# Optimization experiments

Hardware: AMD Instinct MI355X
Metric: run time of the kernel (lower is better)

Reference implementation:

```python
import jax, jax.numpy as jnp
import numpy as np

N_NODES = 49
FEAT_DIM = 1280            # efficientnet_v2_s feature dim
NODE_DIM = FEAT_DIM // N_NODES  # 26
GAT_HID = 256
HEADS = 4
NUM_CLASSES = 5
BATCH = 8192


def _grid_edges():
    # 7x7 grid, 8-neighborhood, as in _create_grid_edges, plus PyG default self loops
    edges = []
    for i in range(7):
        for j in range(7):
            node = i * 7 + j
            for di in (-1, 0, 1):
                for dj in (-1, 0, 1):
                    if di == 0 and dj == 0:
                        continue
                    ni, nj = i + di, j + dj
                    if 0 <= ni < 7 and 0 <= nj < 7:
                        edges.append((node, ni * 7 + nj))
    edges += [(n, n) for n in range(N_NODES)]  # add_self_loops=True (PyG default)
    return np.asarray(edges, dtype=np.int64).T  # [2, 361]


def setup_inputs() -> dict:
    key = jax.random.key(0)
    ks = jax.random.split(key, 16)
    s = 0.05
    inp = {
        "x": jax.random.normal(ks[0], (BATCH, FEAT_DIM), jnp.float32),
        "transform_w": jax.random.normal(ks[1], (FEAT_DIM, N_NODES * NODE_DIM), jnp.float32) * s,
        "transform_b": jnp.zeros((N_NODES * NODE_DIM,), jnp.float32),
        # GATv2 layer 1: 26 -> 64 per head, 4 heads, concat -> 256
        "g1_wl": jax.random.normal(ks[2], (NODE_DIM, GAT_HID), jnp.float32) * s,
        "g1_wr": jax.random.normal(ks[3], (NODE_DIM, GAT_HID), jnp.float32) * s,
        "g1_att": jax.random.normal(ks[4], (HEADS, GAT_HID // HEADS), jnp.float32) * s,
        "g1_b": jnp.zeros((GAT_HID,), jnp.float32),
        # GATv2 layer 2: 256 -> 256, 1 head, mean
        "g2_wl": jax.random.normal(ks[5], (GAT_HID, GAT_HID), jnp.float32) * s,
        "g2_wr": jax.random.normal(ks[6], (GAT_HID, GAT_HID), jnp.float32) * s,
        "g2_att": jax.random.normal(ks[7], (1, GAT_HID), jnp.float32) * s,
        "g2_b": jnp.zeros((GAT_HID,), jnp.float32),
        "fc_w": jax.random.normal(ks[8], (NODE_DIM + GAT_HID, NUM_CLASSES), jnp.float32) * s,
        "fc_b": jnp.zeros((NUM_CLASSES,), jnp.float32),
        "edge_index": jnp.asarray(_grid_edges()),
    }
    return inp


def _gatv2(x, src, dst, wl, wr, att, b, heads, out_ch, concat):
    # PyG GATv2Conv (share_weights=False, negative_slope=0.2, eval mode)
    n = x.shape[0]
    xl = (x @ wl).reshape(n, heads, out_ch)  # source messages
    xr = (x @ wr).reshape(n, heads, out_ch)  # target side of attention
    e = jax.nn.leaky_relu(xl[src] + xr[dst], 0.2)        # [E, H, C]
    score = jnp.einsum('ehc,hc->eh', e, att)             # [E, H]
    smax = jax.ops.segment_max(score, dst, num_segments=n)
    ex = jnp.exp(score - smax[dst])
    den = jax.ops.segment_sum(ex, dst, num_segments=n)
    alpha = ex / den[dst]                                # softmax over in-edges per node
    out = jax.ops.segment_sum(xl[src] * alpha[..., None], dst, num_segments=n)  # [N,H,C]
    out = out.reshape(n, heads * out_ch) if concat else out.mean(axis=1)
    return out + b


def reference(x, transform_w, transform_b, g1_wl, g1_wr, g1_att, g1_b,
              g2_wl, g2_wr, g2_att, g2_b, fc_w, fc_b, edge_index):
    src, dst = edge_index[0], edge_index[1]
    node = (x @ transform_w + transform_b).reshape(-1, N_NODES, NODE_DIM)  # [B,49,26]

    def graph(nf):
        h = _gatv2(nf, src, dst, g1_wl, g1_wr, g1_att, g1_b, HEADS, GAT_HID // HEADS, True)
        h = jax.nn.elu(h)  # dropout inactive in eval
        h = _gatv2(h, src, dst, g2_wl, g2_wr, g2_att, g2_b, 1, GAT_HID, False)
        return h  # [49, 256]

    g = jax.vmap(graph)(node)                              # [B,49,256]
    pooled = jnp.concatenate([node, g], axis=-1).mean(axis=1)  # [B, 282]
    return pooled @ fc_w + fc_b
```

## Files before the change

### kernel.cpp

```cpp
#include <hip/hip_runtime.h>
#include <hip/hip_bf16.h>

typedef __bf16 bf16;
typedef __attribute__((ext_vector_type(8))) __bf16 bf16x8;
typedef __attribute__((ext_vector_type(4))) __bf16 bf16x4;
typedef __attribute__((ext_vector_type(4))) float f32x4;

constexpr int BATCH = 8192, NN = 49, ND = 26, NOUT = 1274, FD = 1280;
constexpr int HID = 256, NE = 361, HEADS = 4;
constexpr int KT_X = 40;
constexpr int MT_X = 512;
constexpr int NB_W = 10;
constexpr int NTB  = 9;

constexpr size_t OFF_XPACK = 0;
constexpr size_t SZ_XPACK  = (size_t)MT_X * KT_X * 512 * 2;
constexpr size_t OFF_WPACK = OFF_XPACK + SZ_XPACK;
constexpr size_t SZ_WPACK  = (size_t)NB_W * NTB * KT_X * 512 * 2;
constexpr size_t OFF_B1    = OFF_WPACK + SZ_WPACK;
constexpr size_t SZ_B1     = (size_t)32 * 512 * 2;
constexpr size_t OFF_B2    = OFF_B1 + SZ_B1;
constexpr size_t SZ_B2     = (size_t)32 * 8 * 512 * 2;
constexpr size_t OFF_N32   = OFF_B2 + SZ_B2;
constexpr size_t SZ_N32    = (size_t)BATCH * NN * 32 * 2;
constexpr size_t OFF_PN    = OFF_N32 + SZ_N32;
constexpr size_t SZ_PN     = (size_t)BATCH * ND * 4;
constexpr size_t OFF_CSR   = OFF_PN + SZ_PN;
constexpr size_t SZ_CSR    = 8192;
constexpr size_t OFF_CHUNK = OFF_CSR + SZ_CSR;


__global__ __launch_bounds__(256) void k_pack_x(const float* __restrict__ x,
                                                bf16* __restrict__ xp) {
    int g = blockIdx.x * 256 + threadIdx.x;
    int lane = g & 63, frag = g >> 6;
    int mt = frag / KT_X, kt = frag - mt * KT_X;
    int row = mt * 16 + (lane & 15);
    int k0  = kt * 32 + (lane >> 4) * 8;
    const float* src = x + (size_t)row * FD + k0;
    bf16x8 v;
#pragma unroll
    for (int j = 0; j < 8; ++j) v[j] = (bf16)src[j];
    *(bf16x8*)(xp + ((size_t)frag * 64 + lane) * 8) = v;
}

__global__ __launch_bounds__(256) void k_pack_w(const float* __restrict__ w,
                                                bf16* __restrict__ wp) {
    int g = blockIdx.x * 256 + threadIdx.x;
    int lane = g & 63, frag = g >> 6;
    int kt = frag % KT_X, t2 = frag / KT_X;
    int nt = t2 % NTB, nb = t2 / NTB;
    int col = nb * 130 + nt * 16 + (lane & 15);
    int k0  = kt * 32 + (lane >> 4) * 8;
    bool ok = (col < NOUT) && (col < nb * 130 + 130);
    bf16x8 v;
#pragma unroll
    for (int j = 0; j < 8; ++j)
        v[j] = ok ? (bf16)w[(size_t)(k0 + j) * NOUT + col] : (bf16)0.f;
    *(bf16x8*)(wp + ((size_t)frag * 64 + lane) * 8) = v;
}

__global__ __launch_bounds__(256) void k_pack_g1(const float* __restrict__ wl,
                                                 const float* __restrict__ wr,
                                                 bf16* __restrict__ bp) {
    int g = blockIdx.x * 256 + threadIdx.x;
    int lane = g & 63, nt = g >> 6;
    int n  = nt * 16 + (lane & 15);
    int k0 = (lane >> 4) * 8;
    bf16x8 v;
#pragma unroll
    for (int j = 0; j < 8; ++j) {
        int k = k0 + j;
        float f = 0.f;
        if (k < ND) f = (n < HID) ? wl[k * HID + n] : wr[k * HID + (n - HID)];
        v[j] = (bf16)f;
    }
    *(bf16x8*)(bp + ((size_t)nt * 64 + lane) * 8) = v;
}

__global__ __launch_bounds__(256) void k_pack_g2(const float* __restrict__ wl,
                                                 const float* __restrict__ wr,
                                                 bf16* __restrict__ bp) {
    int g = blockIdx.x * 256 + threadIdx.x;
    int lane = g & 63, frag = g >> 6;
    int nt = frag >> 3, kt = frag & 7;
    int n  = nt * 16 + (lane & 15);
    int k0 = kt * 32 + (lane >> 4) * 8;
    bf16x8 v;
#pragma unroll
    for (int j = 0; j < 8; ++j) {
        int k = k0 + j;
        float f = (n < HID) ? wl[k * HID + n] : wr[k * HID + (n - HID)];
        v[j] = (bf16)f;
    }
    *(bf16x8*)(bp + ((size_t)frag * 64 + lane) * 8) = v;
}

__global__ __launch_bounds__(128) void k_csr_par(const int* __restrict__ ei,
                                                 int* __restrict__ csr) {
    __shared__ int es[NE], ed[NE], cnt[NN], ocnt[NN], off[NN + 1], ooff[NN + 1];
    int tid = threadIdx.x;
    if (tid < NN) { cnt[tid] = 0; ocnt[tid] = 0; }
    for (int e = tid; e < NE; e += 128) { es[e] = ei[e]; ed[e] = ei[NE + e]; }
    __syncthreads();
    for (int e = tid; e < NE; e += 128) {
        atomicAdd(&cnt[ed[e]], 1);
        atomicAdd(&ocnt[es[e]], 1);
    }
    __syncthreads();
    if (tid == 0) {
        off[0] = 0; ooff[0] = 0;
        for (int n = 0; n < NN; ++n) {
            off[n + 1] = off[n] + cnt[n];
            ooff[n + 1] = ooff[n] + ocnt[n];
        }
    }
    __syncthreads();
    if (tid < NN) {
        int p = off[tid];
        for (int e = 0; e < NE; ++e)
            if (ed[e] == tid) { csr[50 + p] = e; csr[411 + p] = es[e]; ++p; }
    } else if (tid >= 64 && tid < 64 + NN) {
        int n = tid - 64;
        int p = ooff[n];
        for (int e = 0; e < NE; ++e)
            if (es[e] == n) { csr[822 + p] = e; ++p; }
    }
    if (tid < 50) { csr[tid] = off[tid]; csr[772 + tid] = ooff[tid]; }
}

__global__ __launch_bounds__(256, 2) void k_gemm_node(const bf16* __restrict__ xp,
                                                      const bf16* __restrict__ wp,
                                                      const float* __restrict__ tb,
                                                      bf16* __restrict__ node32) {
    __shared__ bf16 L[128][148];
    __shared__ float tbS[144];
    int tid = threadIdx.x, lane = tid & 63, w = tid >> 6;
    int nb = blockIdx.y, C0 = nb * 130;
    int mt0 = blockIdx.x * 16 + w * 4;
    if (tid < 144) { int col = C0 + tid; tbS[tid] = (col < NOUT) ? tb[col] : 0.f; }
    f32x4 acc[4][9] = {};
    const bf16* wpB = wp + (size_t)(nb * NTB) * KT_X * 512;
    for (int kt = 0; kt < KT_X; ++kt) {
        bf16x8 a[4];
#pragma unroll
        for (int i = 0; i < 4; ++i)
            a[i] = *(const bf16x8*)(xp + (((size_t)(mt0 + i) * KT_X + kt) * 64 + lane) * 8);
#pragma unroll
        for (int j = 0; j < NTB; ++j) {
            bf16x8 b = *(const bf16x8*)(wpB + ((size_t)(j * KT_X + kt) * 64 + lane) * 8);
#pragma unroll
            for (int i = 0; i < 4; ++i)
                acc[i][j] = __builtin_amdgcn_mfma_f32_16x16x32_bf16(a[i], b, acc[i][j], 0, 0, 0);
        }
    }
    int c0 = lane & 15, r0 = (lane >> 4) * 4;
    int nodes = (nb == 9) ? 4 : 5;
    int total = 128 * nodes * 4;
    for (int half = 0; half < 2; ++half) {
        __syncthreads();
        if ((w >> 1) == half) {
            int lrbase = (w & 1) * 64;
#pragma unroll
            for (int i = 0; i < 4; ++i) {
#pragma unroll
                for (int j = 0; j < NTB; ++j) {
                    int col = j * 16 + c0;
                    float bias = tbS[col];
#pragma unroll
                    for (int r = 0; r < 4; ++r)
                        L[lrbase + i * 16 + r0 + r][col] = (bf16)(acc[i][j][r] + bias);
                }
            }
        }
        __syncthreads();
        int B0 = blockIdx.x * 256 + half * 128;
        for (int t = tid; t < total; t += 256) {
            int q = t & 3, t2 = t >> 2;
            int n_l = t2 % nodes, brow = t2 / nodes;
            bf16x8 o;
#pragma unroll
            for (int jj = 0; jj < 8; ++jj) {
                int d = q * 8 + jj;
                o[jj] = (d < ND) ? L[brow][n_l * 26 + d] : (bf16)0.f;
            }
            *(bf16x8*)(node32 + (((size_t)(B0 + brow) * NN + nb * 5 + n_l) * 32 + q * 8)) = o;
        }
    }
}

__global__ __launch_bounds__(256) void k_pool(const bf16* __restrict__ node32,
                                              float* __restrict__ pN) {
    int b = blockIdx.x * 8 + (threadIdx.x >> 5);
    int d = threadIdx.x & 31;
    if (d >= ND) return;
    const bf16* base = node32 + (size_t)b * NN * 32 + d;
    float s = 0.f;
    for (int n = 0; n < NN; ++n) s += (float)base[n * 32];
    pN[b * ND + d] = s;
}

__global__ __launch_bounds__(512, 2) void k_fuse1(const bf16* __restrict__ n32,
                                                  const bf16* __restrict__ B1p,
                                                  bf16* __restrict__ h1f,
                                                  const float* __restrict__ att1,
                                                  const float* __restrict__ g1b,
                                                  const int* __restrict__ ei,
                                                  const int* __restrict__ csr) {
    __shared__ __align__(16) char X[NN * 1024];
    __shared__ __align__(16) float attS[256];
    __shared__ float sc[NE * 4], srden[NN * 4], bS[256];
    __shared__ int ieOff[50], ieId[NE], ieSrc[NE], srcS[NE], dstS[NE];

    int tid = threadIdx.x, lane = tid & 63, w = tid >> 6, g = blockIdx.x;

    for (int i = tid; i < 256; i += 512) { attS[i] = att1[i]; bS[i] = g1b[i]; }
    for (int i = tid; i < NE; i += 512) {
        srcS[i] = ei[i]; dstS[i] = ei[NE + i];
        ieId[i] = csr[50 + i]; ieSrc[i] = csr[411 + i];
    }
    if (tid < 50) ieOff[tid] = csr[tid];

    {
        int mt = w & 3, ng = w >> 2;
        int m = mt * 16 + (lane & 15);
        bf16x8 bfrag = {};
        if (m < NN)
            bfrag = *(const bf16x8*)(n32 + ((size_t)(g * NN + m) * 32 + (lane >> 4) * 8));
        int chq = (lane >> 4) * 4;
        int sw = (m & 7) << 4;
        char* rowp = X + m * 1024;
#pragma unroll
        for (int j = 0; j < 16; ++j) {
            f32x4 z = {0.f, 0.f, 0.f, 0.f};
            bf16x8 afrag = *(const bf16x8*)(B1p + ((size_t)(ng * 16 + j) * 64 + lane) * 8);
            f32x4 acc = __builtin_amdgcn_mfma_f32_16x16x32_bf16(afrag, bfrag, z, 0, 0, 0);
            if (m < NN) {
                int ch = (ng * 16 + j) * 16 + chq;
                bf16x4 o4;
#pragma unroll
                for (int r = 0; r < 4; ++r) o4[r] = (bf16)acc[r];
                *(bf16x4*)(rowp + ((ch * 2) ^ sw)) = o4;
            }
        }
    }
    __syncthreads();

    int rot = tid & 7;
    for (int task = tid; task < NE * 4; task += 512) {
        int h = task / NE, e = task - h * NE;
        int s = srcS[e], d = dstS[e];
        int sws = (s & 7) << 4, swd = (d & 7) << 4;
        const char* ps = X + s * 1024;
        const char* pd = X + d * 1024;
        float pa[4] = {0.f, 0.f, 0.f, 0.f};
#pragma unroll
        for (int i = 0; i < 8; ++i) {
            int cc = ((i + rot) & 7) * 8;
            bf16x8 xl = *(const bf16x8*)(ps + (((h * 64 + cc) * 2) ^ sws));
            bf16x8 xr = *(const bf16x8*)(pd + (((256 + h * 64 + cc) * 2) ^ swd));
            float4 a0 = *(const float4*)(attS + h * 64 + cc);
            float4 a1 = *(const float4*)(attS + h * 64 + cc + 4);
            const float aa[8] = {a0.x, a0.y, a0.z, a0.w, a1.x, a1.y, a1.z, a1.w};
#pragma unroll
            for (int q = 0; q < 8; ++q) {
                float v = (float)xl[q] + (float)xr[q];
                v = v > 0.f ? v : 0.2f * v;
                pa[q & 3] = fmaf(aa[q], v, pa[q & 3]);
            }
        }
        sc[e * 4 + h] = (pa[0] + pa[1]) + (pa[2] + pa[3]);
    }
    __syncthreads();
    for (int t = tid; t < NN * 4; t += 512) {
        int n = t >> 2, h = t & 3;
        float m = -1e30f;
        for (int j = ieOff[n]; j < ieOff[n + 1]; ++j) m = fmaxf(m, sc[ieId[j] * 4 + h]);
        float den = 0.f;
        for (int j = ieOff[n]; j < ieOff[n + 1]; ++j) {
            int idx = ieId[j] * 4 + h;
            float ex = __expf(sc[idx] - m);
            sc[idx] = ex; den += ex;
        }
        srden[t] = 1.f / den;
    }
    __syncthreads();
    for (int task = tid; task < NN * 32; task += 512) {
        int n = task >> 5, cb = task & 31;
        int ch0 = cb * 8, hh = cb >> 3;
        float a8[8] = {};
        int j0 = ieOff[n], j1 = ieOff[n + 1];
        for (int j = j0; j < j1; ++j) {
            float al = sc[ieId[j] * 4 + hh];
            int s = ieSrc[j];
            bf16x8 xv = *(const bf16x8*)(X + s * 1024 + ((ch0 * 2) ^ ((s & 7) << 4)));
#pragma unroll
            for (int q = 0; q < 8; ++q) a8[q] = fmaf(al, (float)xv[q], a8[q]);
        }
        float rs = srden[n * 4 + hh];
        bf16x8 o;
#pragma unroll
        for (int q = 0; q < 8; ++q) {
            float v = fmaf(a8[q], rs, bS[ch0 + q]);
            v = v > 0.f ? v : (__expf(v) - 1.f);
            o[q] = (bf16)v;
        }
        int Rl = g * NN + n;
        int kt = ch0 >> 5, kg = (ch0 >> 3) & 3;
        size_t addr = (((size_t)(Rl >> 4) * 8 + kt) * 64 + (Rl & 15) + 16 * kg) * 8;
        *(bf16x8*)(h1f + addr) = o;
    }
}

__global__ __launch_bounds__(256) void k_gemm_l2(const bf16* __restrict__ Af,
                                                 const bf16* __restrict__ Bf,
                                                 bf16* __restrict__ xlr) {
    __shared__ bf16 LT[128][136];
    int tid = threadIdx.x, lane = tid & 63, w = tid >> 6;
    int mtb = blockIdx.x * 8 + (w >> 1) * 4;
    int ntb = blockIdx.y * 8 + (w & 1) * 4;
    f32x4 acc[4][4] = {};
    for (int kt = 0; kt < 8; ++kt) {
        bf16x8 a[4], b[4];
#pragma unroll
        for (int i = 0; i < 4; ++i)
            a[i] = *(const bf16x8*)(Af + (((size_t)(mtb + i) * 8 + kt) * 64 + lane) * 8);
#pragma unroll
        for (int j = 0; j < 4; ++j)
            b[j] = *(const bf16x8*)(Bf + (((size_t)(ntb + j) * 8 + kt) * 64 + lane) * 8);
#pragma unroll
        for (int i = 0; i < 4; ++i)
#pragma unroll
            for (int j = 0; j < 4; ++j)
                acc[i][j] = __builtin_amdgcn_mfma_f32_16x16x32_bf16(a[i], b[j], acc[i][j], 0, 0, 0);
    }
    int c0 = lane & 15, r0 = (lane >> 4) * 4;
    int lr0 = (w >> 1) * 64, lc0 = (w & 1) * 64;
#pragma unroll
    for (int i = 0; i < 4; ++i)
#pragma unroll
        for (int j = 0; j < 4; ++j)
#pragma unroll
            for (int r = 0; r < 4; ++r)
                LT[lr0 + i * 16 + r0 + r][lc0 + j * 16 + c0] = (bf16)acc[i][j][r];
    __syncthreads();
    size_t R0 = (size_t)blockIdx.x * 128, C0 = (size_t)blockIdx.y * 128;
#pragma unroll
    for (int it = 0; it < 8; ++it) {
        int idx = (it * 256 + tid) * 8;
        int r = idx >> 7, c = idx & 127;
        bf16x8 v = *(const bf16x8*)&LT[r][c];
        *(bf16x8*)(xlr + (R0 + r) * 512 + C0 + c) = v;
    }
}

__global__ __launch_bounds__(384) void k_score2(const bf16* __restrict__ xlr,
                                                const float* __restrict__ att2,
                                                const int* __restrict__ ei,
                                                float* __restrict__ scE) {
    __shared__ __align__(16) char X[NN * 1024];
    __shared__ float attS[256];
    int tid = threadIdx.x, g = blockIdx.x;
    const char* srcp = (const char*)(xlr + (size_t)g * NN * 512);
    for (int off = tid * 16; off < NN * 1024; off += 384 * 16) {
        int row = off >> 10;
        *(uint4*)(X + (off ^ ((row & 7) << 4))) = *(const uint4*)(srcp + off);
    }
    if (tid < 256) attS[tid] = att2[tid];
    __syncthreads();
    if (tid >= NE) return;
    int s = ei[tid], d = ei[NE + tid];
    int sws = (s & 7) << 4, swd = (d & 7) << 4;
    const char* ps = X + s * 1024;
    const char* pd = X + d * 1024;
    int rot = tid & 7;
    float pa[4] = {0.f, 0.f, 0.f, 0.f};
#pragma unroll 8
    for (int i = 0; i < 32; ++i) {
        int cc = ((i + rot) & 31) * 8;
        bf16x8 xl = *(const bf16x8*)(ps + ((cc * 2) ^ sws));
        bf16x8 xr = *(const bf16x8*)(pd + (((256 + cc) * 2) ^ swd));
        float4 a0 = *(const float4*)(attS + cc);
        float4 a1 = *(const float4*)(attS + cc + 4);
        const float aa[8] = {a0.x, a0.y, a0.z, a0.w, a1.x, a1.y, a1.z, a1.w};
#pragma unroll
        for (int q = 0; q < 8; ++q) {
            float v = (float)xl[q] + (float)xr[q];
            v = v > 0.f ? v : 0.2f * v;
            pa[q & 3] = fmaf(aa[q], v, pa[q & 3]);
        }
    }
    scE[(size_t)g * NE + tid] = (pa[0] + pa[1]) + (pa[2] + pa[3]);
}

__global__ __launch_bounds__(64) void k_softwn(const float* __restrict__ scE,
                                               const int* __restrict__ csr,
                                               const int* __restrict__ ei,
                                               float* __restrict__ wN) {
    __shared__ float sm[NN], sr[NN];
    int g = blockIdx.x, tid = threadIdx.x;
    const float* sg = scE + (size_t)g * NE;
    if (tid < NN) {
        int j0 = csr[tid], j1 = csr[tid + 1];
        float m = -1e30f;
        for (int j = j0; j < j1; ++j) m = fmaxf(m, sg[csr[50 + j]]);
        float den = 0.f;
        for (int j = j0; j < j1; ++j) den += __expf(sg[csr[50 + j]] - m);
        sm[tid] = m; sr[tid] = 1.f / den;
    }
    __syncthreads();
    if (tid < NN) {
        float wa = 0.f;
        int j0 = csr[772 + tid], j1 = csr[772 + tid + 1];
        for (int j = j0; j < j1; ++j) {
            int e = csr[822 + j];
            int d = ei[NE + e];
            wa += __expf(sg[e] - sm[d]) * sr[d];
        }
        wN[(size_t)g * NN + tid] = wa;
    }
}

static __device__ __forceinline__ float waveReduceSum(float v) {
#pragma unroll
    for (int m = 32; m > 0; m >>= 1) v += __shfl_xor(v, m, 64);
    return v;
}

__global__ __launch_bounds__(256) void k_poolfc(const bf16* __restrict__ xlr,
                                                const float* __restrict__ wN,
                                                const float* __restrict__ pN,
                                                const float* __restrict__ g2b,
                                                const float* __restrict__ fcw,
                                                const float* __restrict__ fcb,
                                                int graph_base,
                                                float* __restrict__ out) {
    __shared__ float wSs[NN];
    __shared__ float poolS[288];
    int tid = threadIdx.x, g = blockIdx.x;
    if (tid < NN) wSs[tid] = wN[(size_t)g * NN + tid];
    if (tid >= 64 && tid < 64 + ND)
        poolS[tid - 64] = pN[(size_t)(graph_base + g) * ND + (tid - 64)] * (1.f / NN);
    __syncthreads();
    {
        const bf16* base = xlr + (size_t)g * NN * 512 + tid;
        float acc = 0.f;
        for (int n = 0; n < NN; ++n) acc = fmaf(wSs[n], (float)base[n * 512], acc);
        poolS[ND + tid] = acc * (1.f / NN) + g2b[tid];
    }
    __syncthreads();
    int w5 = tid >> 6, lane = tid & 63;
    for (int o = w5; o < 5; o += 4) {
        float a = 0.f;
        for (int d = lane; d < ND + HID; d += 64) a = fmaf(poolS[d], fcw[d * 5 + o], a);
        a = waveReduceSum(a);
        if (lane == 0) out[(size_t)(graph_base + g) * 5 + o] = a + fcb[o];
    }
}

extern "C" void kernel_launch(void* const* d_in, const int* in_sizes, int n_in,
                              void* d_out, int out_size, void* d_ws, size_t ws_size,
                              hipStream_t stream) {
    const float* x   = (const float*)d_in[0];
    const float* tw  = (const float*)d_in[1];
    const float* tb  = (const float*)d_in[2];
    const float* wl1 = (const float*)d_in[3];
    const float* wr1 = (const float*)d_in[4];
    const float* at1 = (const float*)d_in[5];
    const float* b1  = (const float*)d_in[6];
    const float* wl2 = (const float*)d_in[7];
    const float* wr2 = (const float*)d_in[8];
    const float* at2 = (const float*)d_in[9];
    const float* b2  = (const float*)d_in[10];
    const float* fcw = (const float*)d_in[11];
    const float* fcb = (const float*)d_in[12];
    const int*   ei  = (const int*)d_in[13];
    float* out = (float*)d_out;

    char* ws = (char*)d_ws;
    bf16*  xp   = (bf16*)(ws + OFF_XPACK);
    bf16*  wp   = (bf16*)(ws + OFF_WPACK);
    bf16*  b1p  = (bf16*)(ws + OFF_B1);
    bf16*  b2p  = (bf16*)(ws + OFF_B2);
    bf16*  n32  = (bf16*)(ws + OFF_N32);
    float* pN   = (float*)(ws + OFF_PN);
    int*   csr  = (int*)(ws + OFF_CSR);

    const size_t perC = 50176 + 12544 + 1444 + 196;
    int C = 512;
    for (int cand : {2048, 1024, 512}) {
        if (OFF_CHUNK + (size_t)cand * perC <= ws_size) { C = cand; break; }
    }
    bf16*  xlr = (bf16*)(ws + OFF_CHUNK);
    bf16*  h1f = (bf16*)(ws + OFF_CHUNK + (size_t)C * 50176);
    float* scE = (float*)(ws + OFF_CHUNK + (size_t)C * (50176 + 12544));
    float* wNB = scE + (size_t)C * NE;
    int nchunks = BATCH / C;
    int MtC = C * NN / 16;

    k_pack_x<<<dim3(MT_X * KT_X * 64 / 256), dim3(256), 0, stream>>>(x, xp);
    k_pack_w<<<dim3(NB_W * NTB * KT_X * 64 / 256), dim3(256), 0, stream>>>(tw, wp);
    k_pack_g1<<<dim3(8), dim3(256), 0, stream>>>(wl1, wr1, b1p);
    k_pack_g2<<<dim3(64), dim3(256), 0, stream>>>(wl2, wr2, b2p);
    k_csr_par<<<dim3(1), dim3(128), 0, stream>>>(ei, csr);
    k_gemm_node<<<dim3(32, NB_W), dim3(256), 0, stream>>>(xp, wp, tb, n32);
    k_pool<<<dim3(BATCH / 8), dim3(256), 0, stream>>>(n32, pN);

    for (int c = 0; c < nchunks; ++c) {
        const bf16* n32c = n32 + (size_t)c * C * NN * 32;
        k_fuse1<<<dim3(C), dim3(512), 0, stream>>>(n32c, b1p, h1f, at1, b1, ei, csr);
        k_gemm_l2<<<dim3(MtC / 8, 4), dim3(256), 0, stream>>>(h1f, b2p, xlr);
        k_score2<<<dim3(C), dim3(384), 0, stream>>>(xlr, at2, ei, scE);
        k_softwn<<<dim3(C), dim3(64), 0, stream>>>(scE, csr, ei, wNB);
        k_poolfc<<<dim3(C), dim3(256), 0, stream>>>(xlr, wNB, pN, b2, fcw, fcb,
                                                    c * C, out);
    }
}
```

Baseline: 944.0 us.

## Aggregate layer-1 attention via dense MFMA matrix and fuse softmax into score2

```diff
diff --git a/kernel.cpp b/kernel.cpp
--- a/kernel.cpp
+++ b/kernel.cpp
@@ -119,7 +119,7 @@
     if (tid < NN) {
         int p = off[tid];
         for (int e = 0; e < NE; ++e)
-            if (ed[e] == tid) { csr[50 + p] = e; csr[411 + p] = es[e]; ++p; }
+            if (ed[e] == tid) { csr[50 + p] = e; csr[411 + p] = es[e]; csr[1200 + p] = tid; ++p; }
     } else if (tid >= 64 && tid < 64 + NN) {
         int n = tid - 64;
         int p = ooff[n];
@@ -205,19 +205,18 @@
                                                   bf16* __restrict__ h1f,
                                                   const float* __restrict__ att1,
                                                   const float* __restrict__ g1b,
-                                                  const int* __restrict__ ei,
                                                   const int* __restrict__ csr) {
     __shared__ __align__(16) char X[NN * 1024];
+    __shared__ __align__(16) bf16 P2[2][64][72];
     __shared__ __align__(16) float attS[256];
-    __shared__ float sc[NE * 4], srden[NN * 4], bS[256];
-    __shared__ int ieOff[50], ieId[NE], ieSrc[NE], srcS[NE], dstS[NE];
+    __shared__ float sc2[NE * 2], bS[256];
+    __shared__ int ieOff[50], ieDst[NE], ieSrc[NE];
 
     int tid = threadIdx.x, lane = tid & 63, w = tid >> 6, g = blockIdx.x;
 
     for (int i = tid; i < 256; i += 512) { attS[i] = att1[i]; bS[i] = g1b[i]; }
     for (int i = tid; i < NE; i += 512) {
-        srcS[i] = ei[i]; dstS[i] = ei[NE + i];
-        ieId[i] = csr[50 + i]; ieSrc[i] = csr[411 + i];
+        ieDst[i] = csr[1200 + i]; ieSrc[i] = csr[411 + i];
     }
     if (tid < 50) ieOff[tid] = csr[tid];
 
@@ -246,62 +245,97 @@
     }
     __syncthreads();
 
-    int rot = tid & 7;
-    for (int task = tid; task < NE * 4; task += 512) {
-        int h = task / NE, e = task - h * NE;
-        int s = srcS[e], d = dstS[e];
-        int sws = (s & 7) << 4, swd = (d & 7) << 4;
-        const char* ps = X + s * 1024;
-        const char* pd = X + d * 1024;
-        float pa[4] = {0.f, 0.f, 0.f, 0.f};
-#pragma unroll
-        for (int i = 0; i < 8; ++i) {
-            int cc = ((i + rot) & 7) * 8;
-            bf16x8 xl = *(const bf16x8*)(ps + (((h * 64 + cc) * 2) ^ sws));
-            bf16x8 xr = *(const bf16x8*)(pd + (((256 + h * 64 + cc) * 2) ^ swd));
-            float4 a0 = *(const float4*)(attS + h * 64 + cc);
-            float4 a1 = *(const float4*)(attS + h * 64 + cc + 4);
-            const float aa[8] = {a0.x, a0.y, a0.z, a0.w, a1.x, a1.y, a1.z, a1.w};
-#pragma unroll
-            for (int q = 0; q < 8; ++q) {
-                float v = (float)xl[q] + (float)xr[q];
-                v = v > 0.f ? v : 0.2f * v;
-                pa[q & 3] = fmaf(aa[q], v, pa[q & 3]);
-            }
-        }
-        sc[e * 4 + h] = (pa[0] + pa[1]) + (pa[2] + pa[3]);
-    }
-    __syncthreads();
-    for (int t = tid; t < NN * 4; t += 512) {
-        int n = t >> 2, h = t & 3;
-        float m = -1e30f;
-        for (int j = ieOff[n]; j < ieOff[n + 1]; ++j) m = fmaxf(m, sc[ieId[j] * 4 + h]);
-        float den = 0.f;
-        for (int j = ieOff[n]; j < ieOff[n + 1]; ++j) {
-            int idx = ieId[j] * 4 + h;
-            float ex = __expf(sc[idx] - m);
-            sc[idx] = ex; den += ex;
-        }
-        srden[t] = 1.f / den;
+    f32x4 agg[2][4] = {};
+    int lhw = w >> 2, ntw = w & 3;
+    int chw = ntw * 16 + (lane & 15);
+
+#pragma unroll
+    for (int hp = 0; hp < 2; ++hp) {
+        {
+            uint4 z4 = {0u, 0u, 0u, 0u};
+            for (int t = tid; t < 1152; t += 512) ((uint4*)P2)[t] = z4;
+        }
+        int rot = tid & 7;
+        for (int t = tid; t < NE * 2; t += 512) {
+            int j = t >> 1, lh = t & 1, h = hp * 2 + lh;
+            int s = ieSrc[j], d = ieDst[j];
+            int sws = (s & 7) << 4, swd = (d & 7) << 4;
+            const char* ps = X + s * 1024;
+            const char* pd = X + d * 1024;
+            float pa[4] = {0.f, 0.f, 0.f, 0.f};
+#pragma unroll
+            for (int i = 0; i < 8; ++i) {
+                int cc = ((i + rot) & 7) * 8;
+                bf16x8 xl = *(const bf16x8*)(ps + (((h * 64 + cc) * 2) ^ sws));
+                bf16x8 xr = *(const bf16x8*)(pd + (((256 + h * 64 + cc) * 2) ^ swd));
+                float4 a0 = *(const float4*)(attS + h * 64 + cc);
+                float4 a1 = *(const float4*)(attS + h * 64 + cc + 4);
+                const float aa[8] = {a0.x, a0.y, a0.z, a0.w, a1.x, a1.y, a1.z, a1.w};
+#pragma unroll
+                for (int q = 0; q < 8; ++q) {
+                    float v = (float)xl[q] + (float)xr[q];
+                    v = v > 0.f ? v : 0.2f * v;
+                    pa[q & 3] = fmaf(aa[q], v, pa[q & 3]);
+                }
+            }
+            sc2[t] = (pa[0] + pa[1]) + (pa[2] + pa[3]);
+        }
+        __syncthreads();
+        for (int t = tid; t < NN * 2; t += 512) {
+            int n = t >> 1, lh = t & 1;
+            int j0 = ieOff[n], j1 = ieOff[n + 1];
+            float m = -1e30f;
+            for (int j = j0; j < j1; ++j) m = fmaxf(m, sc2[j * 2 + lh]);
+            float den = 0.f;
+            for (int j = j0; j < j1; ++j) den += __expf(sc2[j * 2 + lh] - m);
+            float r = 1.f / den;
+            for (int j = j0; j < j1; ++j)
+                P2[lh][n][ieSrc[j]] = (bf16)(__expf(sc2[j * 2 + lh] - m) * r);
+        }
+        __syncthreads();
+        {
+            int h = hp * 2 + lhw;
+#pragma unroll
+            for (int ks = 0; ks < 2; ++ks) {
+                bf16x8 bb;
+#pragma unroll
+                for (int j2 = 0; j2 < 8; ++j2) {
+                    int k = ks * 32 + ((lane >> 4) << 3) + j2;
+                    int kk = (k < NN) ? k : 0;
+                    bb[j2] = *(const bf16*)(X + kk * 1024 + (((h * 64 + chw) * 2) ^ ((kk & 7) << 4)));
+                }
+#pragma unroll
+                for (int mt = 0; mt < 4; ++mt) {
+                    bf16x8 aa = *(const bf16x8*)(&P2[lhw][mt * 16 + (lane & 15)][ks * 32 + ((lane >> 4) << 3)]);
+                    agg[hp][mt] = __builtin_amdgcn_mfma_f32_16x16x32_bf16(aa, bb, agg[hp][mt], 0, 0, 0);
+                }
+            }
+        }
+        __syncthreads();
+    }
+
+#pragma unroll
+    for (int hp = 0; hp < 2; ++hp) {
+        int ch256 = (hp * 2 + lhw) * 64 + chw;
+#pragma unroll
+        for (int mt = 0; mt < 4; ++mt) {
+#pragma unroll
+            for (int r = 0; r < 4; ++r) {
+                int n = mt * 16 + ((lane >> 4) << 2) + r;
+                if (n < NN)
+                    *(bf16*)(X + n * 1024 + (((256 + ch256) * 2) ^ ((n & 7) << 4))) = (bf16)agg[hp][mt][r];
+            }
+        }
     }
     __syncthreads();
     for (int task = tid; task < NN * 32; task += 512) {
         int n = task >> 5, cb = task & 31;
-        int ch0 = cb * 8, hh = cb >> 3;
-        float a8[8] = {};
-        int j0 = ieOff[n], j1 = ieOff[n + 1];
-        for (int j = j0; j < j1; ++j) {
-            float al = sc[ieId[j] * 4 + hh];
-            int s = ieSrc[j];
-            bf16x8 xv = *(const bf16x8*)(X + s * 1024 + ((ch0 * 2) ^ ((s & 7) << 4)));
-#pragma unroll
-            for (int q = 0; q < 8; ++q) a8[q] = fmaf(al, (float)xv[q], a8[q]);
-        }
-        float rs = srden[n * 4 + hh];
+        int ch0 = cb * 8;
+        bf16x8 xv = *(const bf16x8*)(X + n * 1024 + (((256 + ch0) * 2) ^ ((n & 7) << 4)));
         bf16x8 o;
 #pragma unroll
         for (int q = 0; q < 8; ++q) {
-            float v = fmaf(a8[q], rs, bS[ch0 + q]);
+            float v = (float)xv[q] + bS[ch0 + q];
             v = v > 0.f ? v : (__expf(v) - 1.f);
             o[q] = (bf16)v;
         }
@@ -357,9 +391,11 @@
 __global__ __launch_bounds__(384) void k_score2(const bf16* __restrict__ xlr,
                                                 const float* __restrict__ att2,
                                                 const int* __restrict__ ei,
-                                                float* __restrict__ scE) {
+                                                const int* __restrict__ csr,
+                                                float* __restrict__ wN) {
     __shared__ __align__(16) char X[NN * 1024];
     __shared__ float attS[256];
+    __shared__ float sc[NE], sm[NN], sr[NN];
     int tid = threadIdx.x, g = blockIdx.x;
     const char* srcp = (const char*)(xlr + (size_t)g * NN * 512);
     for (int off = tid * 16; off < NN * 1024; off += 384 * 16) {
@@ -368,44 +404,37 @@
     }
     if (tid < 256) attS[tid] = att2[tid];
     __syncthreads();
-    if (tid >= NE) return;
-    int s = ei[tid], d = ei[NE + tid];
-    int sws = (s & 7) << 4, swd = (d & 7) << 4;
-    const char* ps = X + s * 1024;
-    const char* pd = X + d * 1024;
-    int rot = tid & 7;
-    float pa[4] = {0.f, 0.f, 0.f, 0.f};
+    if (tid < NE) {
+        int s = ei[tid], d = ei[NE + tid];
+        int sws = (s & 7) << 4, swd = (d & 7) << 4;
+        const char* ps = X + s * 1024;
+        const char* pd = X + d * 1024;
+        int rot = tid & 7;
+        float pa[4] = {0.f, 0.f, 0.f, 0.f};
 #pragma unroll 8
-    for (int i = 0; i < 32; ++i) {
-        int cc = ((i + rot) & 31) * 8;
-        bf16x8 xl = *(const bf16x8*)(ps + ((cc * 2) ^ sws));
-        bf16x8 xr = *(const bf16x8*)(pd + (((256 + cc) * 2) ^ swd));
-        float4 a0 = *(const float4*)(attS + cc);
-        float4 a1 = *(const float4*)(attS + cc + 4);
-        const float aa[8] = {a0.x, a0.y, a0.z, a0.w, a1.x, a1.y, a1.z, a1.w};
-#pragma unroll
-        for (int q = 0; q < 8; ++q) {
-            float v = (float)xl[q] + (float)xr[q];
-            v = v > 0.f ? v : 0.2f * v;
-            pa[q & 3] = fmaf(aa[q], v, pa[q & 3]);
-        }
-    }
-    scE[(size_t)g * NE + tid] = (pa[0] + pa[1]) + (pa[2] + pa[3]);
-}
-
-__global__ __launch_bounds__(64) void k_softwn(const float* __restrict__ scE,
-                                               const int* __restrict__ csr,
-                                               const int* __restrict__ ei,
-                                               float* __restrict__ wN) {
-    __shared__ float sm[NN], sr[NN];
-    int g = blockIdx.x, tid = threadIdx.x;
-    const float* sg = scE + (size_t)g * NE;
+        for (int i = 0; i < 32; ++i) {
+            int cc = ((i + rot) & 31) * 8;
+            bf16x8 xl = *(const bf16x8*)(ps + ((cc * 2) ^ sws));
+            bf16x8 xr = *(const bf16x8*)(pd + (((256 + cc) * 2) ^ swd));
+            float4 a0 = *(const float4*)(attS + cc);
+            float4 a1 = *(const float4*)(attS + cc + 4);
+            const float aa[8] = {a0.x, a0.y, a0.z, a0.w, a1.x, a1.y, a1.z, a1.w};
+#pragma unroll
+            for (int q = 0; q < 8; ++q) {
+                float v = (float)xl[q] + (float)xr[q];
+                v = v > 0.f ? v : 0.2f * v;
+                pa[q & 3] = fmaf(aa[q], v, pa[q & 3]);
+            }
+        }
+        sc[tid] = (pa[0] + pa[1]) + (pa[2] + pa[3]);
+    }
+    __syncthreads();
     if (tid < NN) {
         int j0 = csr[tid], j1 = csr[tid + 1];
         float m = -1e30f;
-        for (int j = j0; j < j1; ++j) m = fmaxf(m, sg[csr[50 + j]]);
+        for (int j = j0; j < j1; ++j) m = fmaxf(m, sc[csr[50 + j]]);
         float den = 0.f;
-        for (int j = j0; j < j1; ++j) den += __expf(sg[csr[50 + j]] - m);
+        for (int j = j0; j < j1; ++j) den += __expf(sc[csr[50 + j]] - m);
         sm[tid] = m; sr[tid] = 1.f / den;
     }
     __syncthreads();
@@ -415,7 +444,7 @@
         for (int j = j0; j < j1; ++j) {
             int e = csr[822 + j];
             int d = ei[NE + e];
-            wa += __expf(sg[e] - sm[d]) * sr[d];
+            wa += __expf(sc[e] - sm[d]) * sr[d];
         }
         wN[(size_t)g * NN + tid] = wa;
     }
@@ -486,15 +515,14 @@
     float* pN   = (float*)(ws + OFF_PN);
     int*   csr  = (int*)(ws + OFF_CSR);
 
-    const size_t perC = 50176 + 12544 + 1444 + 196;
+    const size_t perC = 50176 + 12544 + 196;
     int C = 512;
     for (int cand : {2048, 1024, 512}) {
         if (OFF_CHUNK + (size_t)cand * perC <= ws_size) { C = cand; break; }
     }
     bf16*  xlr = (bf16*)(ws + OFF_CHUNK);
     bf16*  h1f = (bf16*)(ws + OFF_CHUNK + (size_t)C * 50176);
-    float* scE = (float*)(ws + OFF_CHUNK + (size_t)C * (50176 + 12544));
-    float* wNB = scE + (size_t)C * NE;
+    float* wNB = (float*)(ws + OFF_CHUNK + (size_t)C * (50176 + 12544));
     int nchunks = BATCH / C;
     int MtC = C * NN / 16;
 
@@ -508,10 +536,9 @@
 
     for (int c = 0; c < nchunks; ++c) {
         const bf16* n32c = n32 + (size_t)c * C * NN * 32;
-        k_fuse1<<<dim3(C), dim3(512), 0, stream>>>(n32c, b1p, h1f, at1, b1, ei, csr);
+        k_fuse1<<<dim3(C), dim3(512), 0, stream>>>(n32c, b1p, h1f, at1, b1, csr);
         k_gemm_l2<<<dim3(MtC / 8, 4), dim3(256), 0, stream>>>(h1f, b2p, xlr);
-        k_score2<<<dim3(C), dim3(384), 0, stream>>>(xlr, at2, ei, scE);
-        k_softwn<<<dim3(C), dim3(64), 0, stream>>>(scE, csr, ei, wNB);
+        k_score2<<<dim3(C), dim3(384), 0, stream>>>(xlr, at2, ei, csr, wNB);
         k_poolfc<<<dim3(C), dim3(256), 0, stream>>>(xlr, wNB, pN, b2, fcw, fcb,
                                                     c * C, out);
     }
```

After: 978.0 us. 3.6% more time.

## Fuse layer-2 score, softmax weights, and pooling/FC into one kernel

Applied to the files above, without the earlier changes.

```diff
diff --git a/kernel.cpp b/kernel.cpp
--- a/kernel.cpp
+++ b/kernel.cpp
@@ -354,12 +354,26 @@
     }
 }
 
-__global__ __launch_bounds__(384) void k_score2(const bf16* __restrict__ xlr,
-                                                const float* __restrict__ att2,
-                                                const int* __restrict__ ei,
-                                                float* __restrict__ scE) {
+static __device__ __forceinline__ float waveReduceSum(float v) {
+#pragma unroll
+    for (int m = 32; m > 0; m >>= 1) v += __shfl_xor(v, m, 64);
+    return v;
+}
+
+__global__ __launch_bounds__(384, 2) void k_post2(const bf16* __restrict__ xlr,
+                                                  const float* __restrict__ att2,
+                                                  const float* __restrict__ pN,
+                                                  const float* __restrict__ g2b,
+                                                  const float* __restrict__ fcw,
+                                                  const float* __restrict__ fcb,
+                                                  const int* __restrict__ ei,
+                                                  const int* __restrict__ csr,
+                                                  int graph_base,
+                                                  float* __restrict__ out) {
     __shared__ __align__(16) char X[NN * 1024];
     __shared__ float attS[256];
+    __shared__ float sc[NE], sm[NN], sr[NN], wS[NN];
+    __shared__ float poolS[288];
     int tid = threadIdx.x, g = blockIdx.x;
     const char* srcp = (const char*)(xlr + (size_t)g * NN * 512);
     for (int off = tid * 16; off < NN * 1024; off += 384 * 16) {
@@ -367,45 +381,40 @@
         *(uint4*)(X + (off ^ ((row & 7) << 4))) = *(const uint4*)(srcp + off);
     }
     if (tid < 256) attS[tid] = att2[tid];
-    __syncthreads();
-    if (tid >= NE) return;
-    int s = ei[tid], d = ei[NE + tid];
-    int sws = (s & 7) << 4, swd = (d & 7) << 4;
-    const char* ps = X + s * 1024;
-    const char* pd = X + d * 1024;
-    int rot = tid & 7;
-    float pa[4] = {0.f, 0.f, 0.f, 0.f};
+    if (tid >= 256 && tid < 256 + ND)
+        poolS[tid - 256] = pN[(size_t)(graph_base + g) * ND + (tid - 256)] * (1.f / NN);
+    __syncthreads();
+    if (tid < NE) {
+        int s = ei[tid], d = ei[NE + tid];
+        int sws = (s & 7) << 4, swd = (d & 7) << 4;
+        const char* ps = X + s * 1024;
+        const char* pd = X + d * 1024;
+        int rot = tid & 7;
+        float pa[4] = {0.f, 0.f, 0.f, 0.f};
 #pragma unroll 8
-    for (int i = 0; i < 32; ++i) {
-        int cc = ((i + rot) & 31) * 8;
-        bf16x8 xl = *(const bf16x8*)(ps + ((cc * 2) ^ sws));
-        bf16x8 xr = *(const bf16x8*)(pd + (((256 + cc) * 2) ^ swd));
-        float4 a0 = *(const float4*)(attS + cc);
-        float4 a1 = *(const float4*)(attS + cc + 4);
-        const float aa[8] = {a0.x, a0.y, a0.z, a0.w, a1.x, a1.y, a1.z, a1.w};
-#pragma unroll
-        for (int q = 0; q < 8; ++q) {
-            float v = (float)xl[q] + (float)xr[q];
-            v = v > 0.f ? v : 0.2f * v;
-            pa[q & 3] = fmaf(aa[q], v, pa[q & 3]);
-        }
-    }
-    scE[(size_t)g * NE + tid] = (pa[0] + pa[1]) + (pa[2] + pa[3]);
-}
-
-__global__ __launch_bounds__(64) void k_softwn(const float* __restrict__ scE,
-                                               const int* __restrict__ csr,
-                                               const int* __restrict__ ei,
-                                               float* __restrict__ wN) {
-    __shared__ float sm[NN], sr[NN];
-    int g = blockIdx.x, tid = threadIdx.x;
-    const float* sg = scE + (size_t)g * NE;
+        for (int i = 0; i < 32; ++i) {
+            int cc = ((i + rot) & 31) * 8;
+            bf16x8 xl = *(const bf16x8*)(ps + ((cc * 2) ^ sws));
+            bf16x8 xr = *(const bf16x8*)(pd + (((256 + cc) * 2) ^ swd));
+            float4 a0 = *(const float4*)(attS + cc);
+            float4 a1 = *(const float4*)(attS + cc + 4);
+            const float aa[8] = {a0.x, a0.y, a0.z, a0.w, a1.x, a1.y, a1.z, a1.w};
+#pragma unroll
+            for (int q = 0; q < 8; ++q) {
+                float v = (float)xl[q] + (float)xr[q];
+                v = v > 0.f ? v : 0.2f * v;
+                pa[q & 3] = fmaf(aa[q], v, pa[q & 3]);
+            }
+        }
+        sc[tid] = (pa[0] + pa[1]) + (pa[2] + pa[3]);
+    }
+    __syncthreads();
     if (tid < NN) {
         int j0 = csr[tid], j1 = csr[tid + 1];
         float m = -1e30f;
-        for (int j = j0; j < j1; ++j) m = fmaxf(m, sg[csr[50 + j]]);
+        for (int j = j0; j < j1; ++j) m = fmaxf(m, sc[csr[50 + j]]);
         float den = 0.f;
-        for (int j = j0; j < j1; ++j) den += __expf(sg[csr[50 + j]] - m);
+        for (int j = j0; j < j1; ++j) den += __expf(sc[csr[50 + j]] - m);
         sm[tid] = m; sr[tid] = 1.f / den;
     }
     __syncthreads();
@@ -415,46 +424,27 @@
         for (int j = j0; j < j1; ++j) {
             int e = csr[822 + j];
             int d = ei[NE + e];
-            wa += __expf(sg[e] - sm[d]) * sr[d];
-        }
-        wN[(size_t)g * NN + tid] = wa;
-    }
-}
-
-static __device__ __forceinline__ float waveReduceSum(float v) {
-#pragma unroll
-    for (int m = 32; m > 0; m >>= 1) v += __shfl_xor(v, m, 64);
-    return v;
-}
-
-__global__ __launch_bounds__(256) void k_poolfc(const bf16* __restrict__ xlr,
-                                                const float* __restrict__ wN,
-                                                const float* __restrict__ pN,
-                                                const float* __restrict__ g2b,
-                                                const float* __restrict__ fcw,
-                                                const float* __restrict__ fcb,
-                                                int graph_base,
-                                                float* __restrict__ out) {
-    __shared__ float wSs[NN];
-    __shared__ float poolS[288];
-    int tid = threadIdx.x, g = blockIdx.x;
-    if (tid < NN) wSs[tid] = wN[(size_t)g * NN + tid];
-    if (tid >= 64 && tid < 64 + ND)
-        poolS[tid - 64] = pN[(size_t)(graph_base + g) * ND + (tid - 64)] * (1.f / NN);
-    __syncthreads();
-    {
-        const bf16* base = xlr + (size_t)g * NN * 512 + tid;
+            wa += __expf(sc[e] - sm[d]) * sr[d];
+        }
+        wS[tid] = wa;
+    }
+    __syncthreads();
+    if (tid < HID) {
         float acc = 0.f;
-        for (int n = 0; n < NN; ++n) acc = fmaf(wSs[n], (float)base[n * 512], acc);
+#pragma unroll
+        for (int n = 0; n < NN; ++n) {
+            float v = (float)*(const bf16*)(X + n * 1024 + ((tid * 2) ^ ((n & 7) << 4)));
+            acc = fmaf(wS[n], v, acc);
+        }
         poolS[ND + tid] = acc * (1.f / NN) + g2b[tid];
     }
     __syncthreads();
     int w5 = tid >> 6, lane = tid & 63;
-    for (int o = w5; o < 5; o += 4) {
+    if (w5 < 5) {
         float a = 0.f;
-        for (int d = lane; d < ND + HID; d += 64) a = fmaf(poolS[d], fcw[d * 5 + o], a);
+        for (int d = lane; d < ND + HID; d += 64) a = fmaf(poolS[d], fcw[d * 5 + w5], a);
         a = waveReduceSum(a);
-        if (lane == 0) out[(size_t)(graph_base + g) * 5 + o] = a + fcb[o];
+        if (lane == 0) out[(size_t)(graph_base + g) * 5 + w5] = a + fcb[w5];
     }
 }
 
@@ -486,15 +476,13 @@
     float* pN   = (float*)(ws + OFF_PN);
     int*   csr  = (int*)(ws + OFF_CSR);
 
-    const size_t perC = 50176 + 12544 + 1444 + 196;
+    const size_t perC = 50176 + 12544;
     int C = 512;
     for (int cand : {2048, 1024, 512}) {
         if (OFF_CHUNK + (size_t)cand * perC <= ws_size) { C = cand; break; }
     }
     bf16*  xlr = (bf16*)(ws + OFF_CHUNK);
     bf16*  h1f = (bf16*)(ws + OFF_CHUNK + (size_t)C * 50176);
-    float* scE = (float*)(ws + OFF_CHUNK + (size_t)C * (50176 + 12544));
-    float* wNB = scE + (size_t)C * NE;
     int nchunks = BATCH / C;
     int MtC = C * NN / 16;
 
@@ -510,9 +498,7 @@
         const bf16* n32c = n32 + (size_t)c * C * NN * 32;
         k_fuse1<<<dim3(C), dim3(512), 0, stream>>>(n32c, b1p, h1f, at1, b1, ei, csr);
         k_gemm_l2<<<dim3(MtC / 8, 4), dim3(256), 0, stream>>>(h1f, b2p, xlr);
-        k_score2<<<dim3(C), dim3(384), 0, stream>>>(xlr, at2, ei, scE);
-        k_softwn<<<dim3(C), dim3(64), 0, stream>>>(scE, csr, ei, wNB);
-        k_poolfc<<<dim3(C), dim3(256), 0, stream>>>(xlr, wNB, pN, b2, fcw, fcb,
-                                                    c * C, out);
-    }
-}
+        k_post2<<<dim3(C), dim3(384), 0, stream>>>(xlr, at2, pN, b2, fcw, fcb,
+                                                   ei, csr, c * C, out);
+    }
+}
```

New measurement: 959.2 us. Within noise of the previous version (+1.6%).
